# Kernel tuning notes

Measured on AMD Instinct MI355X. Metric: run time of the kernel, lower is better.

Reference implementation:

```python
import jax, jax.numpy as jnp
import numpy as np
import math

B, L, IN_K, IN_V = 4, 2048, 256, 256
HID, HEADS, OUT = 1024, 8, 256
D = HID // HEADS  # head_dim = 128


def setup_inputs() -> dict:
    key = jax.random.key(0)
    ks = jax.random.split(key, 9)
    s = 0.02
    return {
        "KEY": jax.random.normal(ks[0], (B, L, IN_K), jnp.float32),
        "VALUE": jax.random.normal(ks[1], (B, L, IN_V), jnp.float32),
        "QUERY": jax.random.normal(ks[2], (B, L, IN_K), jnp.float32),
        "W_w": jax.random.normal(ks[3], (HID, IN_K), jnp.float32) * s,
        "W_b": jax.random.normal(ks[4], (HID,), jnp.float32) * s,
        "Wv_w": jax.random.normal(ks[5], (HID, IN_V), jnp.float32) * s,
        "Wv_b": jax.random.normal(ks[6], (HID,), jnp.float32) * s,
        "Wo_w": jax.random.normal(ks[7], (OUT, HID), jnp.float32) * s,
        "Wo_b": jax.random.normal(ks[8], (OUT,), jnp.float32) * s,
    }


def _split_heads(x, b, l):
    # reshape hidden -> (head_dim, num_heads) [head LAST, as in source], then
    # permute(0,3,1,2) -> [B, heads, L, head_dim]
    return x.reshape(b, l, D, HEADS).transpose(0, 3, 1, 2)


def reference(KEY, VALUE, QUERY, W_w, W_b, Wv_w, Wv_b, Wo_w, Wo_b):
    b, lk, _ = KEY.shape
    lq = QUERY.shape[1]
    # shared projection W for KEY and QUERY
    Wk = _split_heads(KEY @ W_w.T + W_b, b, lk)      # [B,h,Lk,d]
    Wq = _split_heads(QUERY @ W_w.T + W_b, b, lq)    # [B,h,Lq,d]
    Wv = _split_heads(VALUE @ Wv_w.T + Wv_b, b, lk)  # [B,h,Lk,d]
    # score[b,h,i,k] = sum_j Wk[b,h,i,j] * Wq[b,h,k,j]
    score = jnp.einsum('bhij,bhkj->bhik', Wk, Wq) / math.sqrt(D)
    # NON-STANDARD: softmax over the HEAD dimension (dim=1)
    attn = jax.nn.softmax(score, axis=1)             # [B,h,Lk,Lq]
    out = jnp.einsum('bhik,bhij->bhjk', attn, Wv)    # [B,h,d,Lq]
    out = out.transpose(0, 2, 1, 3)                  # [B,d,h,Lq]
    out = out.reshape(b, D * HEADS, lq)              # [B,hidden,Lq]
    out = jnp.swapaxes(out, 2, 1)                    # [B,Lq,hidden]
    # dropout is identity in eval mode
    return out @ Wo_w.T + Wo_b                       # [B,Lq,output_size]
```

## Files before the change

kernel.cpp:

```cpp
#include <hip/hip_runtime.h>
#include <hip/hip_bf16.h>
#include <stdint.h>

#define B_    4
#define L_    2048
#define INK   256
#define HID   1024
#define NH    8
#define DH    128
#define OUTF  256

typedef __bf16 v8bf __attribute__((ext_vector_type(8)));
typedef float  v4f  __attribute__((ext_vector_type(4)));

#define MFMA(a,b,c) __builtin_amdgcn_mfma_f32_16x16x32_bf16((a),(b),(c),0,0,0)

__device__ __forceinline__ void gl_lds16(const void* gsrc, void* ldsbase) {
  __builtin_amdgcn_global_load_lds(
      (const __attribute__((address_space(1))) unsigned int*)(uintptr_t)gsrc,
      (__attribute__((address_space(3))) unsigned int*)(uint32_t)(uintptr_t)ldsbase,
      16, 0, 0);
}
__device__ __forceinline__ void sched_fence() { asm volatile("" ::: "memory"); }
__device__ __forceinline__ void barrier_lgkm() {
  asm volatile("s_waitcnt lgkmcnt(0)\n\ts_barrier" ::: "memory");
}

__device__ __forceinline__ unsigned short bfbits(float f) {
  __bf16 h = (__bf16)f;
  return __builtin_bit_cast(unsigned short, h);
}
__device__ __forceinline__ unsigned pack2(float a, float b) {
  return (unsigned)bfbits(a) | ((unsigned)bfbits(b) << 16);
}

struct ConvArgs {
  const float* src[5];
  __bf16* dst[5];
  int n[5];
};
__global__ __launch_bounds__(256)
void convert_kernel(ConvArgs a) {
  const int r = blockIdx.y;
  const int i = (blockIdx.x * 256 + threadIdx.x) * 4;
  if (i >= a.n[r]) return;
  const float4 v = *(const float4*)(a.src[r] + i);
  uint2 w;
  w.x = pack2(v.x, v.y);
  w.y = pack2(v.z, v.w);
  *reinterpret_cast<uint2*>(a.dst[r] + i) = w;
}

__global__ __launch_bounds__(256)
void wo_perm_kernel(const float* __restrict__ Wo, __bf16* __restrict__ Wop) {
  const int o = blockIdx.x;
  const int hidp = threadIdx.x * 4;
  const int h = hidp >> 7, dd = hidp & 127;
  const float* src = Wo + (size_t)o * HID;
  const float v0 = src[(dd + 0) * 8 + h];
  const float v1 = src[(dd + 1) * 8 + h];
  const float v2 = src[(dd + 2) * 8 + h];
  const float v3 = src[(dd + 3) * 8 + h];
  uint2 w;
  w.x = pack2(v0, v1);
  w.y = pack2(v2, v3);
  *reinterpret_cast<uint2*>(Wop + (size_t)o * HID + hidp) = w;
}

template<int MODE>
__global__ __launch_bounds__(256, 2)
void proj_kernel(const __bf16* __restrict__ X, const __bf16* __restrict__ W,
                 const float* __restrict__ bias, __bf16* __restrict__ out)
{
  __shared__ __bf16 sA[2][128 * 64];
  __shared__ __bf16 sB[2][128 * 64];
  const int tid  = threadIdx.x;
  const int lane = tid & 63;
  const int wid  = tid >> 6;
  const int l15  = lane & 15;
  const int q    = lane >> 4;
  const int mblk = blockIdx.x * 128;
  const int nblk = blockIdx.y * 128;

  v4f acc[4][4];
  const v4f vz = {0.f, 0.f, 0.f, 0.f};
#pragma unroll
  for (int i = 0; i < 4; i++)
#pragma unroll
    for (int j = 0; j < 4; j++) acc[i][j] = vz;

  const char* Ab = (const char*)X + (size_t)mblk * 512;
  const char* Bb = (const char*)W + (size_t)nblk * 512;

  auto stage = [&](int p, int c) {
    const int koff = c * 128;
#pragma unroll
    for (int j = 0; j < 4; j++) {
      const int slot = j * 256 + tid;
      const int row = slot >> 3, g = slot & 7;
      gl_lds16(Ab + (size_t)row * 512 + koff + ((g ^ (row & 7)) << 4),
               &sA[p][(j * 256 + wid * 64) * 8]);
    }
#pragma unroll
    for (int j = 0; j < 4; j++) {
      const int slot = j * 256 + tid;
      const int row = slot >> 3, g = slot & 7;
      gl_lds16(Bb + (size_t)row * 512 + koff + ((g ^ (row & 7)) << 4),
               &sB[p][(j * 256 + wid * 64) * 8]);
    }
  };

  stage(0, 0);
  __syncthreads();
#pragma unroll
  for (int c = 0; c < 4; c++) {
    const int p = c & 1;
    if (c + 1 < 4) stage(1 - p, c + 1);
#pragma unroll
    for (int s = 0; s < 2; s++) {
      v8bf a[4], b[4];
#pragma unroll
      for (int t = 0; t < 4; t++) {
        const int row = (wid & 1) * 64 + t * 16 + l15;
        a[t] = *(const v8bf*)&sA[p][(row << 6) + (((s * 4 + q) ^ (row & 7)) << 3)];
      }
#pragma unroll
      for (int t = 0; t < 4; t++) {
        const int row = (wid >> 1) * 64 + t * 16 + l15;
        b[t] = *(const v8bf*)&sB[p][(row << 6) + (((s * 4 + q) ^ (row & 7)) << 3)];
      }
#pragma unroll
      for (int tm = 0; tm < 4; tm++)
#pragma unroll
        for (int tn = 0; tn < 4; tn++)
          acc[tm][tn] = MFMA(a[tm], b[tn], acc[tm][tn]);
    }
    __syncthreads();
  }

#pragma unroll
  for (int tn = 0; tn < 4; tn++) {
    const int n = nblk + (wid >> 1) * 64 + tn * 16 + l15;
    const float bv = bias[n];
    const int h = n & 7;
    const int dd = n >> 3;
#pragma unroll
    for (int tm = 0; tm < 4; tm++)
#pragma unroll
      for (int r = 0; r < 4; r++) {
        const int m = mblk + (wid & 1) * 64 + tm * 16 + q * 4 + r;
        const int b = m >> 11;
        const int i = m & (L_ - 1);
        const float v = acc[tm][tn][r] + bv;
        size_t idx;
        if (MODE == 0) {
          idx = ((size_t)(b * NH + h) * L_ + i) * DH + dd;
        } else {
          const int ii = (i >> 3) & 3;
          idx = ((size_t)(b * NH + h) * 64 + (i >> 5)) * 4096 +
                (ii * 128 + (dd ^ (ii << 1))) * 8 + (i & 7);
        }
        out[idx] = (__bf16)v;
      }
  }
}

__global__ __launch_bounds__(512, 2)
void fused_attn_kernel(const __bf16* __restrict__ Kp,
                       const __bf16* __restrict__ Qp,
                       const __bf16* __restrict__ Vg,
                       __bf16* __restrict__ Hd)
{
  extern __shared__ char smem[];
  char* sV = smem;
  char* sP = smem + 131072;

  const int tid  = threadIdx.x;
  const int lane = tid & 63;
  const int h    = tid >> 6;
  const int l15  = lane & 15;
  const int q    = lane >> 4;
  const int k0   = blockIdx.x * 32;
  const int b    = blockIdx.y;

  const char* KpH = (const char*)Kp + (size_t)(b * NH + h) * L_ * DH * 2;
  const char* QpH = (const char*)Qp + (size_t)(b * NH + h) * L_ * DH * 2;
  const char* VgH = (const char*)Vg + (size_t)(b * NH + h) * 64 * 8192;
  char* sPh = sP + h * 2560;

  auto stage_V = [&](int p, int i0) {
    char* sVp = sV + p * 65536 + h * 8192;
    const char* src = VgH + (size_t)(i0 >> 5) * 8192;
#pragma unroll
    for (int j = 0; j < 8; j++)
      gl_lds16(src + (j * 64 + lane) * 16, sVp + j * 1024);
  };
  auto loadKa = [&](v8bf (&ka)[2][4], int i0) {
#pragma unroll
    for (int si = 0; si < 2; si++)
#pragma unroll
      for (int c = 0; c < 4; c++)
        ka[si][c] = *(const v8bf*)(KpH + (size_t)(i0 + si * 16 + l15) * 256 + (c * 4 + q) * 16);
  };

  v8bf qf[2][4];
  v8bf kaE[2][4], kaO[2][4];

  stage_V(0, 0);
  sched_fence();
  loadKa(kaE, 0);
#pragma unroll
  for (int n = 0; n < 2; n++)
#pragma unroll
    for (int c = 0; c < 4; c++)
      qf[n][c] = *(const v8bf*)(QpH + (size_t)(k0 + n * 16 + l15) * 256 + c * 64 + q * 16);
  stage_V(1, 32);
  sched_fence();
  loadKa(kaO, 32);

  v4f cacc[8][2];
  const v4f vz = {0.f, 0.f, 0.f, 0.f};
#pragma unroll
  for (int t = 0; t < 8; t++)
#pragma unroll
    for (int n = 0; n < 2; n++) cacc[t][n] = vz;

  const float c2 = 0.12751744f;
  const int ip = tid & 15;
  const int kk = tid >> 4;

  auto phase = [&](v8bf (&ka)[2][4], int bufp, int i0, bool pf) {
    v4f s[2][2];
#pragma unroll
    for (int si = 0; si < 2; si++)
#pragma unroll
      for (int n = 0; n < 2; n++) s[si][n] = vz;
#pragma unroll
    for (int c = 0; c < 4; c++)
#pragma unroll
      for (int si = 0; si < 2; si++)
#pragma unroll
        for (int n = 0; n < 2; n++)
          s[si][n] = MFMA(ka[si][c], qf[n][c], s[si][n]);

#pragma unroll
    for (int si = 0; si < 2; si++)
#pragma unroll
      for (int n = 0; n < 2; n++) {
        const float p0 = exp2f(s[si][n][0] * c2);
        const float p1 = exp2f(s[si][n][1] * c2);
        const float p2 = exp2f(s[si][n][2] * c2);
        const float p3 = exp2f(s[si][n][3] * c2);
        uint2 w;
        w.x = pack2(p0, p1);
        w.y = pack2(p2, p3);
        *(uint2*)(sPh + (n * 16 + l15) * 80 + (si * 16 + q * 4) * 2) = w;
      }
    barrier_lgkm();

    {
      unsigned u[8];
      float lo[8], hi[8], s0 = 0.f, s1 = 0.f;
#pragma unroll
      for (int hh = 0; hh < 8; hh++)
        u[hh] = *(const unsigned*)(sP + hh * 2560 + kk * 80 + ip * 4);
#pragma unroll
      for (int hh = 0; hh < 8; hh++) {
        lo[hh] = __builtin_bit_cast(float, u[hh] << 16);
        hi[hh] = __builtin_bit_cast(float, u[hh] & 0xFFFF0000u);
        s0 += lo[hh];
        s1 += hi[hh];
      }
      const float r0 = __builtin_amdgcn_rcpf(s0);
      const float r1 = __builtin_amdgcn_rcpf(s1);
#pragma unroll
      for (int hh = 0; hh < 8; hh++)
        *(unsigned*)(sP + hh * 2560 + kk * 80 + ip * 4) = pack2(lo[hh] * r0, hi[hh] * r1);
    }
    barrier_lgkm();

    char* sVp = sV + bufp * 65536 + h * 8192;
    v8bf va[8], pb[2];
#pragma unroll
    for (int t = 0; t < 8; t++)
      va[t] = *(const v8bf*)(sVp + q * 2048 + (((t * 16 + l15) ^ (q << 1)) << 4));
#pragma unroll
    for (int n = 0; n < 2; n++)
      pb[n] = *(const v8bf*)(sPh + (n * 16 + l15) * 80 + q * 16);

    if (pf) {
      stage_V(bufp, i0 + 64);
      sched_fence();
      loadKa(ka, i0 + 64);
    }

#pragma unroll
    for (int t = 0; t < 8; t++)
#pragma unroll
      for (int n = 0; n < 2; n++)
        cacc[t][n] = MFMA(va[t], pb[n], cacc[t][n]);
  };

#pragma unroll 1
  for (int t = 0; t < 32; t++) {
    phase(kaE, 0, t * 64,      t < 31);
    phase(kaO, 1, t * 64 + 32, t < 31);
  }

#pragma unroll
  for (int t = 0; t < 8; t++)
#pragma unroll
    for (int n = 0; n < 2; n++) {
      uint2 w;
      w.x = pack2(cacc[t][n][0], cacc[t][n][1]);
      w.y = pack2(cacc[t][n][2], cacc[t][n][3]);
      char* dst = (char*)Hd +
          (((size_t)(b * L_ + k0 + n * 16 + l15)) * HID + h * DH + t * 16 + q * 4) * 2;
      *(uint2*)dst = w;
    }
}

__global__ __launch_bounds__(256, 2)
void outproj_kernel(const __bf16* __restrict__ Hd, const __bf16* __restrict__ Wop,
                    const float* __restrict__ bo, float* __restrict__ out)
{
  __shared__ __bf16 sA[2][64 * 64];
  __shared__ __bf16 sB[2][64 * 64];
  const int tid  = threadIdx.x;
  const int lane = tid & 63;
  const int wid  = tid >> 6;
  const int l15  = lane & 15;
  const int q    = lane >> 4;
  const int mblk = blockIdx.x * 64;
  const int nblk = blockIdx.y * 64;

  const char* Ab = (const char*)Hd  + (size_t)mblk * 2048;
  const char* Bb = (const char*)Wop + (size_t)nblk * 2048;

  auto stage = [&](int p, int c) {
#pragma unroll
    for (int j = 0; j < 2; j++) {
      const int slot = j * 256 + tid;
      const int row = slot >> 3, g = slot & 7;
      gl_lds16(Ab + (size_t)row * 2048 + c * 128 + ((g ^ (row & 7)) << 4),
               &sA[p][(j * 256 + wid * 64) * 8]);
    }
#pragma unroll
    for (int j = 0; j < 2; j++) {
      const int slot = j * 256 + tid;
      const int row = slot >> 3, g = slot & 7;
      gl_lds16(Bb + (size_t)row * 2048 + c * 128 + ((g ^ (row & 7)) << 4),
               &sB[p][(j * 256 + wid * 64) * 8]);
    }
  };

  v4f acc[2][2];
  const v4f vz = {0.f, 0.f, 0.f, 0.f};
#pragma unroll
  for (int i = 0; i < 2; i++)
#pragma unroll
    for (int j = 0; j < 2; j++) acc[i][j] = vz;

  stage(0, 0);
  __syncthreads();
#pragma unroll 1
  for (int c = 0; c < 16; c++) {
    const int p = c & 1;
    if (c + 1 < 16) stage(1 - p, c + 1);
#pragma unroll
    for (int s = 0; s < 2; s++) {
      v8bf a[2], bb[2];
#pragma unroll
      for (int t = 0; t < 2; t++) {
        const int row = (wid & 1) * 32 + t * 16 + l15;
        a[t] = *(const v8bf*)&sA[p][(row << 6) + (((s * 4 + q) ^ (row & 7)) << 3)];
      }
#pragma unroll
      for (int t = 0; t < 2; t++) {
        const int row = (wid >> 1) * 32 + t * 16 + l15;
        bb[t] = *(const v8bf*)&sB[p][(row << 6) + (((s * 4 + q) ^ (row & 7)) << 3)];
      }
#pragma unroll
      for (int tm = 0; tm < 2; tm++)
#pragma unroll
        for (int tn = 0; tn < 2; tn++)
          acc[tm][tn] = MFMA(a[tm], bb[tn], acc[tm][tn]);
    }
    __syncthreads();
  }

#pragma unroll
  for (int tn = 0; tn < 2; tn++) {
    const int n = nblk + (wid >> 1) * 32 + tn * 16 + l15;
    const float bv = bo[n];
#pragma unroll
    for (int tm = 0; tm < 2; tm++)
#pragma unroll
      for (int r = 0; r < 4; r++) {
        const int m = mblk + (wid & 1) * 32 + tm * 16 + q * 4 + r;
        out[(size_t)m * OUTF + n] = acc[tm][tn][r] + bv;
      }
  }
}

extern "C" void kernel_launch(void* const* d_in, const int* in_sizes, int n_in,
                              void* d_out, int out_size, void* d_ws, size_t ws_size,
                              hipStream_t stream) {
  const float* KEY   = (const float*)d_in[0];
  const float* VALUE = (const float*)d_in[1];
  const float* QUERY = (const float*)d_in[2];
  const float* W_w   = (const float*)d_in[3];
  const float* W_b   = (const float*)d_in[4];
  const float* Wv_w  = (const float*)d_in[5];
  const float* Wv_b  = (const float*)d_in[6];
  const float* Wo_w  = (const float*)d_in[7];
  const float* Wo_b  = (const float*)d_in[8];
  float* out = (float*)d_out;

  const size_t MB = 1024 * 1024;
  char* ws = (char*)d_ws;
  __bf16* Kp  = (__bf16*)(ws);
  __bf16* Qp  = (__bf16*)(ws + 16 * MB);
  __bf16* Vg  = (__bf16*)(ws + 32 * MB);
  __bf16* Hd  = (__bf16*)(ws + 48 * MB);
  __bf16* Wop = (__bf16*)(ws + 64 * MB);
  __bf16* Xk  = (__bf16*)(ws + 48 * MB);
  __bf16* Xq  = (__bf16*)(ws + 48 * MB + 4 * MB);
  __bf16* Xv  = (__bf16*)(ws + 48 * MB + 8 * MB);
  __bf16* Wb  = (__bf16*)(ws + 48 * MB + 12 * MB);
  __bf16* Wvb = (__bf16*)(ws + 48 * MB + 12 * MB + 512 * 1024);

  ConvArgs ca;
  ca.src[0] = KEY;   ca.dst[0] = Xk;  ca.n[0] = B_ * L_ * INK;
  ca.src[1] = QUERY; ca.dst[1] = Xq;  ca.n[1] = B_ * L_ * INK;
  ca.src[2] = VALUE; ca.dst[2] = Xv;  ca.n[2] = B_ * L_ * INK;
  ca.src[3] = W_w;   ca.dst[3] = Wb;  ca.n[3] = HID * INK;
  ca.src[4] = Wv_w;  ca.dst[4] = Wvb; ca.n[4] = HID * INK;
  convert_kernel<<<dim3(2048, 5), 256, 0, stream>>>(ca);
  wo_perm_kernel<<<dim3(256), 256, 0, stream>>>(Wo_w, Wop);

  proj_kernel<0><<<dim3(64, 8), 256, 0, stream>>>(Xk, Wb,  W_b,  Kp);
  proj_kernel<0><<<dim3(64, 8), 256, 0, stream>>>(Xq, Wb,  W_b,  Qp);
  proj_kernel<1><<<dim3(64, 8), 256, 0, stream>>>(Xv, Wvb, Wv_b, Vg);

  fused_attn_kernel<<<dim3(64, B_), 512, 151552, stream>>>(Kp, Qp, Vg, Hd);

  outproj_kernel<<<dim3(128, 4), 256, 0, stream>>>(Hd, Wop, Wo_b, out);
}
```

Baseline: 379.4 us.

## Load V directly to registers, store fp32 probabilities, fold softmax scale into Q

```diff
diff --git a/kernel.cpp b/kernel.cpp
--- a/kernel.cpp
+++ b/kernel.cpp
@@ -70,7 +70,8 @@
 template<int MODE>
 __global__ __launch_bounds__(256, 2)
 void proj_kernel(const __bf16* __restrict__ X, const __bf16* __restrict__ W,
-                 const float* __restrict__ bias, __bf16* __restrict__ out)
+                 const float* __restrict__ bias, float scale,
+                 __bf16* __restrict__ out)
 {
   __shared__ __bf16 sA[2][128 * 64];
   __shared__ __bf16 sB[2][128 * 64];
@@ -151,14 +152,14 @@
         const int m = mblk + (wid & 1) * 64 + tm * 16 + q * 4 + r;
         const int b = m >> 11;
         const int i = m & (L_ - 1);
-        const float v = acc[tm][tn][r] + bv;
+        const float v = (acc[tm][tn][r] + bv) * scale;
         size_t idx;
         if (MODE == 0) {
           idx = ((size_t)(b * NH + h) * L_ + i) * DH + dd;
         } else {
           const int ii = (i >> 3) & 3;
           idx = ((size_t)(b * NH + h) * 64 + (i >> 5)) * 4096 +
-                (ii * 128 + (dd ^ (ii << 1))) * 8 + (i & 7);
+                (ii * 128 + dd) * 8 + (i & 7);
         }
         out[idx] = (__bf16)v;
       }
@@ -172,8 +173,8 @@
                        __bf16* __restrict__ Hd)
 {
   extern __shared__ char smem[];
-  char* sV = smem;
-  char* sP = smem + 131072;
+  char* sPf = smem;
+  char* sPn = smem + 40960;
 
   const int tid  = threadIdx.x;
   const int lane = tid & 63;
@@ -186,37 +187,33 @@
   const char* KpH = (const char*)Kp + (size_t)(b * NH + h) * L_ * DH * 2;
   const char* QpH = (const char*)Qp + (size_t)(b * NH + h) * L_ * DH * 2;
   const char* VgH = (const char*)Vg + (size_t)(b * NH + h) * 64 * 8192;
-  char* sPh = sP + h * 2560;
-
-  auto stage_V = [&](int p, int i0) {
-    char* sVp = sV + p * 65536 + h * 8192;
-    const char* src = VgH + (size_t)(i0 >> 5) * 8192;
-#pragma unroll
-    for (int j = 0; j < 8; j++)
-      gl_lds16(src + (j * 64 + lane) * 16, sVp + j * 1024);
+  char* sPfH = sPf + h * 5120;
+  char* sPnH = sPn + h * 2560;
+
+  auto loadKa = [&](v8bf (&ka)[2][4], int it) {
+    const char* base = KpH + (size_t)it * 32 * 256;
+#pragma unroll
+    for (int si = 0; si < 2; si++)
+#pragma unroll
+      for (int c = 0; c < 4; c++)
+        ka[si][c] = *(const v8bf*)(base + (si * 16 + l15) * 256 + (c * 4 + q) * 16);
   };
-  auto loadKa = [&](v8bf (&ka)[2][4], int i0) {
-#pragma unroll
-    for (int si = 0; si < 2; si++)
-#pragma unroll
-      for (int c = 0; c < 4; c++)
-        ka[si][c] = *(const v8bf*)(KpH + (size_t)(i0 + si * 16 + l15) * 256 + (c * 4 + q) * 16);
+  auto loadVa = [&](v8bf (&va)[8], int it) {
+    const char* base = VgH + (size_t)it * 8192 + q * 2048;
+#pragma unroll
+    for (int t = 0; t < 8; t++)
+      va[t] = *(const v8bf*)(base + (t * 16 + l15) * 16);
   };
 
   v8bf qf[2][4];
-  v8bf kaE[2][4], kaO[2][4];
-
-  stage_V(0, 0);
-  sched_fence();
-  loadKa(kaE, 0);
 #pragma unroll
   for (int n = 0; n < 2; n++)
 #pragma unroll
     for (int c = 0; c < 4; c++)
       qf[n][c] = *(const v8bf*)(QpH + (size_t)(k0 + n * 16 + l15) * 256 + c * 64 + q * 16);
-  stage_V(1, 32);
-  sched_fence();
-  loadKa(kaO, 32);
+
+  v8bf ka[2][4];
+  loadKa(ka, 0);
 
   v4f cacc[8][2];
   const v4f vz = {0.f, 0.f, 0.f, 0.f};
@@ -225,11 +222,15 @@
 #pragma unroll
     for (int n = 0; n < 2; n++) cacc[t][n] = vz;
 
-  const float c2 = 0.12751744f;
   const int ip = tid & 15;
   const int kk = tid >> 4;
 
-  auto phase = [&](v8bf (&ka)[2][4], int bufp, int i0, bool pf) {
+#pragma unroll 1
+  for (int it = 0; it < 64; ++it) {
+    v8bf va[8];
+    loadVa(va, it);
+    sched_fence();
+
     v4f s[2][2];
 #pragma unroll
     for (int si = 0; si < 2; si++)
@@ -243,68 +244,46 @@
         for (int n = 0; n < 2; n++)
           s[si][n] = MFMA(ka[si][c], qf[n][c], s[si][n]);
 
+    if (it + 1 < 64) loadKa(ka, it + 1);
+
 #pragma unroll
     for (int si = 0; si < 2; si++)
 #pragma unroll
       for (int n = 0; n < 2; n++) {
-        const float p0 = exp2f(s[si][n][0] * c2);
-        const float p1 = exp2f(s[si][n][1] * c2);
-        const float p2 = exp2f(s[si][n][2] * c2);
-        const float p3 = exp2f(s[si][n][3] * c2);
-        uint2 w;
-        w.x = pack2(p0, p1);
-        w.y = pack2(p2, p3);
-        *(uint2*)(sPh + (n * 16 + l15) * 80 + (si * 16 + q * 4) * 2) = w;
+        v4f p;
+#pragma unroll
+        for (int r = 0; r < 4; r++) p[r] = exp2f(s[si][n][r]);
+        *(v4f*)(sPfH + (n * 16 + l15) * 160 + si * 64 + q * 16) = p;
       }
     barrier_lgkm();
 
     {
-      unsigned u[8];
-      float lo[8], hi[8], s0 = 0.f, s1 = 0.f;
-#pragma unroll
-      for (int hh = 0; hh < 8; hh++)
-        u[hh] = *(const unsigned*)(sP + hh * 2560 + kk * 80 + ip * 4);
+      float2 vals[8];
+      float s0 = 0.f, s1 = 0.f;
 #pragma unroll
       for (int hh = 0; hh < 8; hh++) {
-        lo[hh] = __builtin_bit_cast(float, u[hh] << 16);
-        hi[hh] = __builtin_bit_cast(float, u[hh] & 0xFFFF0000u);
-        s0 += lo[hh];
-        s1 += hi[hh];
+        vals[hh] = *(const float2*)(sPf + hh * 5120 + kk * 160 + ip * 8);
+        s0 += vals[hh].x;
+        s1 += vals[hh].y;
       }
       const float r0 = __builtin_amdgcn_rcpf(s0);
       const float r1 = __builtin_amdgcn_rcpf(s1);
 #pragma unroll
       for (int hh = 0; hh < 8; hh++)
-        *(unsigned*)(sP + hh * 2560 + kk * 80 + ip * 4) = pack2(lo[hh] * r0, hi[hh] * r1);
+        *(unsigned*)(sPn + hh * 2560 + kk * 80 + ip * 4) =
+            pack2(vals[hh].x * r0, vals[hh].y * r1);
     }
     barrier_lgkm();
 
-    char* sVp = sV + bufp * 65536 + h * 8192;
-    v8bf va[8], pb[2];
-#pragma unroll
-    for (int t = 0; t < 8; t++)
-      va[t] = *(const v8bf*)(sVp + q * 2048 + (((t * 16 + l15) ^ (q << 1)) << 4));
+    v8bf pb[2];
 #pragma unroll
     for (int n = 0; n < 2; n++)
-      pb[n] = *(const v8bf*)(sPh + (n * 16 + l15) * 80 + q * 16);
-
-    if (pf) {
-      stage_V(bufp, i0 + 64);
-      sched_fence();
-      loadKa(ka, i0 + 64);
-    }
-
+      pb[n] = *(const v8bf*)(sPnH + (n * 16 + l15) * 80 + q * 16);
 #pragma unroll
     for (int t = 0; t < 8; t++)
 #pragma unroll
       for (int n = 0; n < 2; n++)
         cacc[t][n] = MFMA(va[t], pb[n], cacc[t][n]);
-  };
-
-#pragma unroll 1
-  for (int t = 0; t < 32; t++) {
-    phase(kaE, 0, t * 64,      t < 31);
-    phase(kaO, 1, t * 64 + 32, t < 31);
   }
 
 #pragma unroll
@@ -439,11 +418,12 @@
   convert_kernel<<<dim3(2048, 5), 256, 0, stream>>>(ca);
   wo_perm_kernel<<<dim3(256), 256, 0, stream>>>(Wo_w, Wop);
 
-  proj_kernel<0><<<dim3(64, 8), 256, 0, stream>>>(Xk, Wb,  W_b,  Kp);
-  proj_kernel<0><<<dim3(64, 8), 256, 0, stream>>>(Xq, Wb,  W_b,  Qp);
-  proj_kernel<1><<<dim3(64, 8), 256, 0, stream>>>(Xv, Wvb, Wv_b, Vg);
-
-  fused_attn_kernel<<<dim3(64, B_), 512, 151552, stream>>>(Kp, Qp, Vg, Hd);
+  const float c2 = 0.12751744f;
+  proj_kernel<0><<<dim3(64, 8), 256, 0, stream>>>(Xk, Wb,  W_b,  1.0f, Kp);
+  proj_kernel<0><<<dim3(64, 8), 256, 0, stream>>>(Xq, Wb,  W_b,  c2,   Qp);
+  proj_kernel<1><<<dim3(64, 8), 256, 0, stream>>>(Xv, Wvb, Wv_b, 1.0f, Vg);
+
+  fused_attn_kernel<<<dim3(64, B_), 512, 61440, stream>>>(Kp, Qp, Vg, Hd);
 
   outproj_kernel<<<dim3(128, 4), 256, 0, stream>>>(Hd, Wop, Wo_b, out);
 }
```

Result: faster. 326.6 us (-13.9%).
